# Kernel tuning notes

Hardware: AMD Instinct MI355X
Metric: run time of the kernel (lower is better)

## Reference

```python
import jax, jax.numpy as jnp
import numpy as np

N, E, F, H, C, B = 50000, 1_600_000, 128, 128, 10, 512


def setup_inputs() -> dict:
    key = jax.random.key(0)
    ks = jax.random.split(key, 12)
    inp = {
        "x": jax.random.normal(ks[0], (N, F), dtype=jnp.float32),
        "edge_index": jax.random.randint(ks[1], (2, E), 0, N, dtype=jnp.int32),
        "batch": jnp.sort(jax.random.randint(ks[2], (N,), 0, B, dtype=jnp.int32)),
        "edge_weight": jax.random.uniform(ks[3], (E,), dtype=jnp.float32),
        "W1": jax.random.normal(ks[4], (F, H), dtype=jnp.float32) * 0.05,
        "b1": jnp.zeros((H,), dtype=jnp.float32),
        "W2": jax.random.normal(ks[5], (H, H), dtype=jnp.float32) * 0.05,
        "b2": jnp.zeros((H,), dtype=jnp.float32),
        "W3": jax.random.normal(ks[6], (H, H), dtype=jnp.float32) * 0.05,
        "b3": jnp.zeros((H,), dtype=jnp.float32),
        "Wlin": jax.random.normal(ks[7], (H, C), dtype=jnp.float32) * 0.05,
        "blin": jnp.zeros((C,), dtype=jnp.float32),
    }
    return inp


def reference(x, edge_index, batch, edge_weight, W1, b1, W2, b2, W3, b3, Wlin, blin):
    n = x.shape[0]
    src, dst = edge_index[0], edge_index[1]
    loops = jnp.arange(n, dtype=src.dtype)
    src_f = jnp.concatenate([src, loops])  # edges + self-loops
    dst_f = jnp.concatenate([dst, loops])

    def make_norm(fill_value):
        # GCN symmetric normalization: D^-1/2 (A + fill*I) D^-1/2 on edge weights
        ew = jnp.concatenate([edge_weight, jnp.full((n,), fill_value, dtype=edge_weight.dtype)])
        deg = jax.ops.segment_sum(ew, dst_f, num_segments=n)
        dinv = jnp.where(deg > 0, deg ** -0.5, 0.0)
        return dinv[src_f] * ew * dinv[dst_f]

    # conv1 was built as GCNConv(in, hidden, out_channels) -> third positional arg is
    # `improved`, truthy => self-loop fill value 2.0; conv2/3 use 1.0.
    norm1 = make_norm(2.0)
    norm = make_norm(1.0)

    def gcn_conv(h, W, b, nrm):
        h = h @ W                                   # [N, H]
        msg = h[src_f] * nrm[:, None]               # [E+N, H] gather
        return jax.ops.segment_sum(msg, dst_f, num_segments=n) + b

    h = jax.nn.relu(gcn_conv(x, W1, b1, norm1))
    h = jax.nn.relu(gcn_conv(h, W2, b2, norm))
    h = gcn_conv(h, W3, b3, norm)

    # global_mean_pool over graph ids
    sums = jax.ops.segment_sum(h, batch, num_segments=B)
    cnt = jax.ops.segment_sum(jnp.ones((n,), dtype=h.dtype), batch, num_segments=B)
    pooled = sums / jnp.maximum(cnt, 1.0)[:, None]

    # dropout is identity in eval mode
    return pooled @ Wlin + blin
```

## Files before the change

### kernel.cpp

```cpp
#include <hip/hip_runtime.h>
#include <hip/hip_fp16.h>

#define F 128
#define HID 128
#define NCLS 10
#define CAP 80
#define NBIN 256
#define NPB 196
#define SCAP 7168
#define EPT 8
#define HLS 136

typedef short short8 __attribute__((ext_vector_type(8)));
typedef float float4v __attribute__((ext_vector_type(4)));
typedef float float2v __attribute__((ext_vector_type(2)));

__device__ __forceinline__ unsigned short f2bf(float f) {
    unsigned int u = __float_as_uint(f);
    unsigned int r = (u + 0x7FFFu + ((u >> 16) & 1u)) >> 16;
    return (unsigned short)r;
}
__device__ __forceinline__ float bf2f(unsigned int h) {
    return __uint_as_float(h << 16);
}
__device__ __forceinline__ unsigned char f2fp8(float a) {
    return (unsigned char)(__builtin_amdgcn_cvt_pk_fp8_f32(a, 0.f, 0, false) & 0xFF);
}

__global__ __launch_bounds__(256) void bin_prep_kernel(
    const int* __restrict__ ei, const float* __restrict__ ew,
    int* __restrict__ gcur, uint2* __restrict__ staging, int E, int nbb,
    const float* __restrict__ W1, const float* __restrict__ W2,
    const float* __restrict__ W3, const float* __restrict__ Wlin,
    const float* __restrict__ blin, const float* __restrict__ b3,
    unsigned short* __restrict__ Wp, unsigned short* __restrict__ Wp3s,
    float* __restrict__ bL) {
    __shared__ int lhist[NBIN];
    __shared__ int lbase[NBIN];
    int tid = threadIdx.x;

    if ((int)blockIdx.x < nbb) {
        lhist[tid] = 0;
        __syncthreads();

        unsigned int rpk[EPT];
        unsigned short rd[EPT];
        unsigned short rloc[EPT];
        int base = blockIdx.x * (256 * EPT);
#pragma unroll
        for (int i = 0; i < EPT; i++) {
            int e = base + tid + i * 256;
            if (e < E) {
                int s = ei[e];
                int d = ei[E + e];
                unsigned int q = (unsigned int)(ew[e] * 65535.0f + 0.5f);
                rpk[i] = (q << 16) | (unsigned int)s;
                rd[i] = (unsigned short)d;
                rloc[i] = (unsigned short)atomicAdd(&lhist[d / NPB], 1);
            } else {
                rpk[i] = 0u; rd[i] = 0; rloc[i] = 0;
            }
        }
        __syncthreads();
        lbase[tid] = atomicAdd(&gcur[tid], lhist[tid]);
        __syncthreads();

#pragma unroll
        for (int i = 0; i < EPT; i++) {
            int e = base + tid + i * 256;
            if (e < E) {
                int bin = (int)rd[i] / NPB;
                int pos = lbase[bin] + (int)rloc[i];
                if (pos < SCAP)
                    staging[(size_t)bin * SCAP + pos] =
                        make_uint2(rpk[i], (unsigned int)rd[i]);
            }
        }
    } else {
        int b = blockIdx.x - nbb;
        if (b < 128) {
            int widx = b >> 6;
            const float* W = (widx == 0) ? W1 : W2;
            int idx = (b & 63) * 256 + tid;
            int j = idx & 7;
            int l = (idx >> 3) & 63;
            int nt = (idx >> 9) & 7;
            int kt = idx >> 12;
            int k = kt * 32 + ((l >> 4) << 3) + j;
            int n = nt * 16 + (l & 15);
            Wp[widx * 16384 + idx] = f2bf(W[k * HID + n]);
        } else if (b < 136) {
            int idx = (b - 128) * 256 + tid;
            int j = idx & 7;
            int l = (idx >> 3) & 63;
            int kt = idx >> 9;
            int k = kt * 32 + ((l >> 4) << 3) + j;
            int n = l & 15;
            float v = 0.f;
            if (n < NCLS) {
                for (int m = 0; m < HID; m++)
                    v += W3[k * HID + m] * Wlin[m * NCLS + n];
            }
            Wp3s[idx] = f2bf(v);
        } else {
            if (tid < NCLS) {
                float bl = blin[tid];
                for (int j = 0; j < HID; j++) bl += b3[j] * Wlin[j * NCLS + tid];
                bL[tid] = bl;
            }
        }
    }
}

__global__ __launch_bounds__(1024, 8) void build_gemm1_kernel(
    const uint2* __restrict__ staging, const int* __restrict__ gcur,
    unsigned int* __restrict__ colw, int* __restrict__ cnt,
    float* __restrict__ dinv1, float* __restrict__ dinv0, int N, int nbins,
    const float* __restrict__ X, const unsigned short* __restrict__ Wp,
    unsigned char* __restrict__ Yb8) {
    __shared__ unsigned int lbuck[NPB * CAP];
    __shared__ int lcnt[NPB];
    int tid = threadIdx.x;

    if ((int)blockIdx.x < nbins) {
        int bin = blockIdx.x;
        int node0 = bin * NPB;

        for (int n = tid; n < NPB; n += 1024) lcnt[n] = 0;
        __syncthreads();

        int bcnt = gcur[bin];
        if (bcnt > SCAP) bcnt = SCAP;
        const uint2* st = staging + (size_t)bin * SCAP;
        for (int i = tid; i < bcnt; i += 1024) {
            uint2 t = st[i];
            int dl = (int)t.y - node0;
            int pos = atomicAdd(&lcnt[dl], 1);
            if (pos < CAP) lbuck[dl * CAP + pos] = t.x;
        }
        __syncthreads();

        for (int it = 0; it < NPB; it += 128) {
            int nl = it + (tid >> 3);
            int lane = tid & 7;
            if (nl < NPB) {
                int gn = node0 + nl;
                if (gn < N) {
                    int c = lcnt[nl];
                    if (c > CAP) c = CAP;
                    float s = 0.f;
                    for (int j = lane; j < c; j += 8)
                        s += (float)(lbuck[nl * CAP + j] >> 16);
                    s += __shfl_down(s, 4, 8);
                    s += __shfl_down(s, 2, 8);
                    s += __shfl_down(s, 1, 8);
                    if (lane == 0) {
                        float deg = s * (1.0f / 65535.0f);
                        cnt[gn] = c;
                        dinv1[gn] = 1.0f / sqrtf(deg + 2.0f);
                        dinv0[gn] = 1.0f / sqrtf(deg + 1.0f);
                    }
                }
            }
        }
        __syncthreads();

        int nvalid = N - node0;
        if (nvalid > NPB) nvalid = NPB;
        if (nvalid <= 0) return;
        int nslots = nvalid * (CAP / 4);
        uint4* dst4 = (uint4*)(colw + (size_t)node0 * CAP);
        const uint4* src4 = (const uint4*)lbuck;
        for (int i = tid; i < nslots; i += 1024) {
            int rowi = i / (CAP / 4);
            int slot = i - rowi * (CAP / 4);
            int c = lcnt[rowi];
            if (c > CAP) c = CAP;
            if (slot * 4 < c) dst4[i] = src4[i];
        }
    } else {
        int tile = blockIdx.x - nbins;
        int wave = tid >> 6, lane = tid & 63;
        int quad = lane >> 4, m = lane & 15;
        int row0 = tile * 256 + wave * 16;
        if (row0 >= N) return;
        int row = row0 + m;
        int rowc = row < N ? row : N - 1;

        short8 a[4];
        const float4* xrow = (const float4*)(X + (size_t)rowc * F);
#pragma unroll
        for (int kt = 0; kt < 4; kt++) {
            float4 p0 = xrow[kt * 8 + quad * 2];
            float4 p1 = xrow[kt * 8 + quad * 2 + 1];
            short8 v;
            v[0] = (short)f2bf(p0.x); v[1] = (short)f2bf(p0.y);
            v[2] = (short)f2bf(p0.z); v[3] = (short)f2bf(p0.w);
            v[4] = (short)f2bf(p1.x); v[5] = (short)f2bf(p1.y);
            v[6] = (short)f2bf(p1.z); v[7] = (short)f2bf(p1.w);
            a[kt] = v;
        }

#pragma unroll
        for (int nt = 0; nt < 8; nt++) {
            float4v c = {0.f, 0.f, 0.f, 0.f};
#pragma unroll
            for (int kt = 0; kt < 4; kt++) {
                short8 b = *(const short8*)(Wp + (((kt * 8 + nt) * 64 + lane) << 3));
                c = __builtin_amdgcn_mfma_f32_16x16x32_bf16(a[kt], b, c, 0, 0, 0);
            }
#pragma unroll
            for (int r = 0; r < 4; r++) {
                int gr = row0 + quad * 4 + r;
                if (gr < N) Yb8[(size_t)gr * HID + nt * 16 + m] = f2fp8(c[r]);
            }
        }
    }
}

__device__ __forceinline__ void agg_edge_q(unsigned int w, int fl,
                                           const uint4* __restrict__ hin4,
                                           float2v acc[8]) {
    uint4 h = hin4[(w & 0xFFFFu) * 8 + fl];
    float f = __half2float(__ushort_as_half((unsigned short)(w >> 16)));
    float2v fv = {f, f};
    acc[0] += fv * __builtin_amdgcn_cvt_pk_f32_fp8(h.x, false);
    acc[1] += fv * __builtin_amdgcn_cvt_pk_f32_fp8(h.x, true);
    acc[2] += fv * __builtin_amdgcn_cvt_pk_f32_fp8(h.y, false);
    acc[3] += fv * __builtin_amdgcn_cvt_pk_f32_fp8(h.y, true);
    acc[4] += fv * __builtin_amdgcn_cvt_pk_f32_fp8(h.z, false);
    acc[5] += fv * __builtin_amdgcn_cvt_pk_f32_fp8(h.z, true);
    acc[6] += fv * __builtin_amdgcn_cvt_pk_f32_fp8(h.w, false);
    acc[7] += fv * __builtin_amdgcn_cvt_pk_f32_fp8(h.w, true);
}

__device__ __forceinline__ void agg_node_fp8(int g, int lane,
                                             const unsigned char* __restrict__ hin,
                                             const unsigned int* __restrict__ colw,
                                             const int* __restrict__ cnt,
                                             const float* __restrict__ dinv,
                                             float fill,
                                             const float* __restrict__ bias,
                                             unsigned short* __restrict__ hl_row) {
    float dv = dinv[g];
    int c = cnt[g];
    if (c > CAP) c = CAP;
    const unsigned int* row = colw + (size_t)g * CAP;
    const uint4* hin4 = (const uint4*)hin;

    unsigned int pk[3];
#pragma unroll
    for (int k = 0; k < 3; k++) {
        int idx = lane + k * 32;
        unsigned int e = (idx < c) ? row[idx] : 0u;
        int s = (int)(e & 0xFFFFu);
        float wf = (float)(e >> 16) * (1.0f / 65535.0f) * dinv[s];
        unsigned short hw = __half_as_ushort(__float2half(wf));
        pk[k] = (e & 0xFFFFu) | ((unsigned int)hw << 16);
    }

    int q = lane >> 3;
    int fl = lane & 7;

    float2v acc[8];
#pragma unroll
    for (int i = 0; i < 8; i++) acc[i] = (float2v){0.f, 0.f};

#pragma unroll
    for (int slot = 0; slot < 3; slot++) {
        int base = slot * 32;
        if (c <= base) break;
        int cc = c - base;
        if (cc > 32) cc = 32;
        for (int jj = 0; jj < cc; jj += 8) {
            unsigned int w0 = (unsigned int)__shfl((int)pk[slot], jj + 2 * q, 32);
            unsigned int w1 = (unsigned int)__shfl((int)pk[slot], jj + 2 * q + 1, 32);
            agg_edge_q(w0, fl, hin4, acc);
            agg_edge_q(w1, fl, hin4, acc);
        }
    }

#pragma unroll
    for (int i = 0; i < 8; i++) {
        acc[i][0] += __shfl_down(acc[i][0], 16, 32);
        acc[i][1] += __shfl_down(acc[i][1], 16, 32);
        acc[i][0] += __shfl_down(acc[i][0], 8, 32);
        acc[i][1] += __shfl_down(acc[i][1], 8, 32);
    }

    if (q == 0) {
        uint4 hv = hin4[(size_t)g * 8 + fl];
        float2v ws = {fill * dv, fill * dv};
        float2v dvv = {dv, dv};
        acc[0] = (acc[0] + ws * __builtin_amdgcn_cvt_pk_f32_fp8(hv.x, false)) * dvv;
        acc[1] = (acc[1] + ws * __builtin_amdgcn_cvt_pk_f32_fp8(hv.x, true)) * dvv;
        acc[2] = (acc[2] + ws * __builtin_amdgcn_cvt_pk_f32_fp8(hv.y, false)) * dvv;
        acc[3] = (acc[3] + ws * __builtin_amdgcn_cvt_pk_f32_fp8(hv.y, true)) * dvv;
        acc[4] = (acc[4] + ws * __builtin_amdgcn_cvt_pk_f32_fp8(hv.z, false)) * dvv;
        acc[5] = (acc[5] + ws * __builtin_amdgcn_cvt_pk_f32_fp8(hv.z, true)) * dvv;
        acc[6] = (acc[6] + ws * __builtin_amdgcn_cvt_pk_f32_fp8(hv.w, false)) * dvv;
        acc[7] = (acc[7] + ws * __builtin_amdgcn_cvt_pk_f32_fp8(hv.w, true)) * dvv;

        const float2v* b2 = (const float2v*)(bias + fl * 16);
        uint4 o0, o1;
        unsigned int ow[8];
#pragma unroll
        for (int i = 0; i < 8; i++) {
            float2v v = acc[i] + b2[i];
            float v0 = fmaxf(v[0], 0.f);
            float v1 = fmaxf(v[1], 0.f);
            ow[i] = (unsigned int)f2bf(v0) | ((unsigned int)f2bf(v1) << 16);
        }
        o0 = make_uint4(ow[0], ow[1], ow[2], ow[3]);
        o1 = make_uint4(ow[4], ow[5], ow[6], ow[7]);
        *(uint4*)(hl_row + fl * 16) = o0;
        *(uint4*)(hl_row + fl * 16 + 8) = o1;
    }
}

__global__ __launch_bounds__(512) void agg_gemm128_kernel(const unsigned char* __restrict__ hin,
                                                          const unsigned int* __restrict__ colw,
                                                          const int* __restrict__ cnt,
                                                          const float* __restrict__ dinv,
                                                          const float* __restrict__ bias,
                                                          const unsigned short* __restrict__ Wp2,
                                                          unsigned char* __restrict__ Yb8,
                                                          int N) {
    __shared__ unsigned short hl[16 * HLS];
    __shared__ unsigned char Ol8[16 * 128];

    int tid = threadIdx.x;
    int gl = tid >> 5, lane = tid & 31;
    int row0 = blockIdx.x * 16;
    int g = row0 + gl;

    if (g < N) {
        agg_node_fp8(g, lane, hin, colw, cnt, dinv, 2.0f, bias, hl + gl * HLS);
    } else if ((lane >> 3) == 0) {
        *(uint4*)(hl + gl * HLS + (lane & 7) * 16) = make_uint4(0u, 0u, 0u, 0u);
        *(uint4*)(hl + gl * HLS + (lane & 7) * 16 + 8) = make_uint4(0u, 0u, 0u, 0u);
    }
    __syncthreads();

    int nt = tid >> 6;
    int lane64 = tid & 63;
    int quad = lane64 >> 4, m = lane64 & 15;

    short8 a[4];
#pragma unroll
    for (int kt = 0; kt < 4; kt++)
        a[kt] = *(const short8*)(hl + m * HLS + kt * 32 + quad * 8);

    float4v c = {0.f, 0.f, 0.f, 0.f};
#pragma unroll
    for (int kt = 0; kt < 4; kt++) {
        short8 b = *(const short8*)(Wp2 + (((kt * 8 + nt) * 64 + lane64) << 3));
        c = __builtin_amdgcn_mfma_f32_16x16x32_bf16(a[kt], b, c, 0, 0, 0);
    }
#pragma unroll
    for (int r = 0; r < 4; r++)
        Ol8[(quad * 4 + r) * 128 + nt * 16 + m] = f2fp8(c[r]);
    __syncthreads();

    if (tid < 128) {
        int gr = row0 + (tid >> 3);
        if (gr < N)
            ((uint4*)(Yb8 + (size_t)gr * 128))[tid & 7] = ((const uint4*)Ol8)[tid];
    }
}

__global__ __launch_bounds__(512) void agg_gemm16_kernel(const unsigned char* __restrict__ hin,
                                                         const unsigned int* __restrict__ colw,
                                                         const int* __restrict__ cnt,
                                                         const float* __restrict__ dinv,
                                                         const float* __restrict__ bias,
                                                         const unsigned short* __restrict__ Wp3s,
                                                         unsigned short* __restrict__ g3s,
                                                         int N) {
    __shared__ unsigned short hl[16 * HLS];

    int tid = threadIdx.x;
    int gl = tid >> 5, lane = tid & 31;
    int row0 = blockIdx.x * 16;
    int g = row0 + gl;

    if (g < N) {
        agg_node_fp8(g, lane, hin, colw, cnt, dinv, 1.0f, bias, hl + gl * HLS);
    } else if ((lane >> 3) == 0) {
        *(uint4*)(hl + gl * HLS + (lane & 7) * 16) = make_uint4(0u, 0u, 0u, 0u);
        *(uint4*)(hl + gl * HLS + (lane & 7) * 16 + 8) = make_uint4(0u, 0u, 0u, 0u);
    }
    __syncthreads();

    if (tid < 64) {
        int lane64 = tid;
        int quad = lane64 >> 4, m = lane64 & 15;
        short8 a[4];
#pragma unroll
        for (int kt = 0; kt < 4; kt++)
            a[kt] = *(const short8*)(hl + m * HLS + kt * 32 + quad * 8);
        float4v c = {0.f, 0.f, 0.f, 0.f};
#pragma unroll
        for (int kt = 0; kt < 4; kt++) {
            short8 b = *(const short8*)(Wp3s + ((kt * 64 + lane64) << 3));
            c = __builtin_amdgcn_mfma_f32_16x16x32_bf16(a[kt], b, c, 0, 0, 0);
        }
#pragma unroll
        for (int r = 0; r < 4; r++) {
            int gr = row0 + quad * 4 + r;
            if (gr < N) g3s[(size_t)gr * 16 + m] = f2bf(c[r]);
        }
    }
}

__device__ __forceinline__ void agg3_slot(unsigned int pk, int cc, int lane2off,
                                          const unsigned short* __restrict__ g3s,
                                          float& ax, float& ay) {
    if (cc == 8) {
        unsigned int w[8];
        unsigned int h[8];
#pragma unroll
        for (int t = 0; t < 8; t++)
            w[t] = (unsigned int)__shfl((int)pk, t, 8);
#pragma unroll
        for (int t = 0; t < 8; t++)
            h[t] = *(const unsigned int*)(g3s + (w[t] & 0xFFFFu) * 16 + lane2off);
#pragma unroll
        for (int t = 0; t < 8; t++) {
            float f = __half2float(__ushort_as_half((unsigned short)(w[t] >> 16)));
            ax += f * bf2f(h[t] & 0xFFFFu);
            ay += f * bf2f(h[t] >> 16);
        }
    } else {
        for (int t = 0; t < cc; t++) {
            unsigned int w = (unsigned int)__shfl((int)pk, t, 8);
            unsigned int h = *(const unsigned int*)(g3s + (w & 0xFFFFu) * 16 + lane2off);
            float f = __half2float(__ushort_as_half((unsigned short)(w >> 16)));
            ax += f * bf2f(h & 0xFFFFu);
            ay += f * bf2f(h >> 16);
        }
    }
}

__global__ __launch_bounds__(256) void agg3_kernel(const unsigned short* __restrict__ g3s,
                                                   const unsigned int* __restrict__ colw,
                                                   const int* __restrict__ cnt,
                                                   const float* __restrict__ dinv,
                                                   unsigned short* __restrict__ h3s, int N) {
    int g = (blockIdx.x * blockDim.x + threadIdx.x) >> 3;
    int lane = threadIdx.x & 7;
    if (g >= N) return;

    float dv = dinv[g];
    int c = cnt[g];
    if (c > CAP) c = CAP;
    const unsigned int* row = colw + (size_t)g * CAP;
    int lane2off = lane * 2;

    unsigned int pk[10];
#pragma unroll
    for (int k = 0; k < 10; k++) {
        int idx = lane + k * 8;
        unsigned int e = (idx < c) ? row[idx] : 0u;
        int s = (int)(e & 0xFFFFu);
        float wf = (float)(e >> 16) * (1.0f / 65535.0f) * dinv[s];
        unsigned short hw = __half_as_ushort(__float2half(wf));
        pk[k] = (e & 0xFFFFu) | ((unsigned int)hw << 16);
    }

    float ax = 0.f, ay = 0.f;
#pragma unroll
    for (int slot = 0; slot < 10; slot++) {
        int base = slot * 8;
        if (c > base) {
            int cc = c - base;
            if (cc > 8) cc = 8;
            agg3_slot(pk[slot], cc, lane2off, g3s, ax, ay);
        }
    }

    unsigned int hv = *(const unsigned int*)(g3s + (size_t)g * 16 + lane2off);
    ax = (ax + dv * bf2f(hv & 0xFFFFu)) * dv;
    ay = (ay + dv * bf2f(hv >> 16)) * dv;

    unsigned int o = (unsigned int)f2bf(ax) | ((unsigned int)f2bf(ay) << 16);
    *(unsigned int*)(h3s + (size_t)g * 16 + lane2off) = o;
}

__global__ __launch_bounds__(256) void pool3_kernel(const unsigned short* __restrict__ h3s,
                                                    const int* __restrict__ batch,
                                                    const float* __restrict__ bL,
                                                    const float* __restrict__ blin,
                                                    float* __restrict__ out, int N, int B) {
    int wave = (blockIdx.x * blockDim.x + threadIdx.x) >> 6;
    int lane = threadIdx.x & 63;
    if (wave >= B) return;
    int g = wave;
    int d = lane & 15, sub = lane >> 4;

    int lo = 0, hi = N;
    while (lo < hi) { int m = (lo + hi) >> 1; if (batch[m] < g) lo = m + 1; else hi = m; }
    int s0 = lo;
    hi = N;
    while (lo < hi) { int m = (lo + hi) >> 1; if (batch[m] < g + 1) lo = m + 1; else hi = m; }
    int s1 = lo;

    float p = 0.f;
    for (int v = s0 + sub; v < s1; v += 4)
        p += bf2f((unsigned int)h3s[(size_t)v * 16 + d]);
    p += __shfl_down(p, 32, 64);
    p += __shfl_down(p, 16, 64);

    if (lane < NCLS) {
        int cntv = s1 - s0;
        float r = (cntv > 0) ? (p / (float)cntv + bL[d]) : blin[d];
        out[g * NCLS + d] = r;
    }
}

extern "C" void kernel_launch(void* const* d_in, const int* in_sizes, int n_in,
                              void* d_out, int out_size, void* d_ws, size_t ws_size,
                              hipStream_t stream) {
    const float* x    = (const float*)d_in[0];
    const int*   ei   = (const int*)d_in[1];
    const int*   batch= (const int*)d_in[2];
    const float* ew   = (const float*)d_in[3];
    const float* W1   = (const float*)d_in[4];
    const float* b1   = (const float*)d_in[5];
    const float* W2   = (const float*)d_in[6];
    const float* b2   = (const float*)d_in[7];
    const float* W3   = (const float*)d_in[8];
    const float* b3   = (const float*)d_in[9];
    const float* Wlin = (const float*)d_in[10];
    const float* blin = (const float*)d_in[11];
    float* out = (float*)d_out;

    int N = in_sizes[0] / F;
    int E = in_sizes[1] / 2;
    int B = out_size / NCLS;

    char* p = (char*)d_ws;
    auto alloc = [&](size_t bytes) -> void* {
        void* r = (void*)p;
        p += (bytes + 255) & ~(size_t)255;
        return r;
    };
    int*            cnt   = (int*)alloc((size_t)N * 4);
    float*          dinv1 = (float*)alloc((size_t)N * 4);
    float*          dinv0 = (float*)alloc((size_t)N * 4);
    int*            gcur  = (int*)alloc(NBIN * 4);
    float*          bL    = (float*)alloc(16 * 4);
    unsigned int*   colw  = (unsigned int*)alloc((size_t)N * CAP * 4);
    unsigned short* Wp    = (unsigned short*)alloc(2 * 16384 * 2);
    unsigned short* Wp3s  = (unsigned short*)alloc(2048 * 2);
    unsigned char*  bufA  = (unsigned char*)alloc((size_t)N * HID);
    unsigned char*  bufB  = (unsigned char*)alloc((size_t)N * HID);
    unsigned short* g3s   = (unsigned short*)alloc((size_t)N * 16 * 2);
    unsigned short* h3s   = (unsigned short*)alloc((size_t)N * 16 * 2);
    uint2*          staging = (uint2*)alloc((size_t)NBIN * SCAP * 8);

    int tb = 256;
    int nbins = (N + NPB - 1) / NPB;
    int nbb = (E + tb * EPT - 1) / (tb * EPT);
    int g1tiles = (N + 255) / 256;

    hipMemsetAsync(gcur, 0, NBIN * 4, stream);
    bin_prep_kernel<<<nbb + 137, tb, 0, stream>>>(ei, ew, gcur, staging, E, nbb,
                                                  W1, W2, W3, Wlin, blin, b3,
                                                  Wp, Wp3s, bL);
    build_gemm1_kernel<<<nbins + g1tiles, 1024, 0, stream>>>(staging, gcur, colw, cnt,
                                                             dinv1, dinv0, N, nbins,
                                                             x, Wp, bufA);

    int fused_blocks = (N + 15) / 16;
    int agg3_blocks = ((N * 8) + tb - 1) / tb;

    agg_gemm128_kernel<<<fused_blocks, 512, 0, stream>>>(bufA, colw, cnt, dinv1, b1,
                                                         Wp + 16384, bufB, N);
    agg_gemm16_kernel<<<fused_blocks, 512, 0, stream>>>(bufB, colw, cnt, dinv0, b2,
                                                        Wp3s, g3s, N);
    agg3_kernel<<<agg3_blocks, tb, 0, stream>>>(g3s, colw, cnt, dinv0, h3s, N);
    pool3_kernel<<<((B * 64) + tb - 1) / tb, tb, 0, stream>>>(h3s, batch, bL, blin,
                                                              out, N, B);
}
```

Baseline: 249.4 us.

## Replace binned staging CSR build with direct atomic scatter into per-node buckets

Result: slower. 339.2 us (+36.0%).

```diff
diff --git a/kernel.cpp b/kernel.cpp
--- a/kernel.cpp
+++ b/kernel.cpp
@@ -5,9 +5,6 @@
 #define HID 128
 #define NCLS 10
 #define CAP 80
-#define NBIN 256
-#define NPB 196
-#define SCAP 7168
 #define EPT 8
 #define HLS 136
 
@@ -27,57 +24,32 @@
     return (unsigned char)(__builtin_amdgcn_cvt_pk_fp8_f32(a, 0.f, 0, false) & 0xFF);
 }
 
-__global__ __launch_bounds__(256) void bin_prep_kernel(
+__global__ __launch_bounds__(256) void scatter_prep_kernel(
     const int* __restrict__ ei, const float* __restrict__ ew,
-    int* __restrict__ gcur, uint2* __restrict__ staging, int E, int nbb,
+    int* __restrict__ cnt, unsigned int* __restrict__ colw, int E, int nsb,
     const float* __restrict__ W1, const float* __restrict__ W2,
     const float* __restrict__ W3, const float* __restrict__ Wlin,
     const float* __restrict__ blin, const float* __restrict__ b3,
     unsigned short* __restrict__ Wp, unsigned short* __restrict__ Wp3s,
     float* __restrict__ bL) {
-    __shared__ int lhist[NBIN];
-    __shared__ int lbase[NBIN];
     int tid = threadIdx.x;
 
-    if ((int)blockIdx.x < nbb) {
-        lhist[tid] = 0;
-        __syncthreads();
-
-        unsigned int rpk[EPT];
-        unsigned short rd[EPT];
-        unsigned short rloc[EPT];
+    if ((int)blockIdx.x < nsb) {
         int base = blockIdx.x * (256 * EPT);
 #pragma unroll
         for (int i = 0; i < EPT; i++) {
-            int e = base + tid + i * 256;
+            int e = base + i * 256 + tid;
             if (e < E) {
                 int s = ei[e];
                 int d = ei[E + e];
                 unsigned int q = (unsigned int)(ew[e] * 65535.0f + 0.5f);
-                rpk[i] = (q << 16) | (unsigned int)s;
-                rd[i] = (unsigned short)d;
-                rloc[i] = (unsigned short)atomicAdd(&lhist[d / NPB], 1);
-            } else {
-                rpk[i] = 0u; rd[i] = 0; rloc[i] = 0;
+                int pos = atomicAdd(&cnt[d], 1);
+                if (pos < CAP)
+                    colw[(size_t)d * CAP + pos] = (q << 16) | (unsigned int)s;
             }
         }
-        __syncthreads();
-        lbase[tid] = atomicAdd(&gcur[tid], lhist[tid]);
-        __syncthreads();
-
-#pragma unroll
-        for (int i = 0; i < EPT; i++) {
-            int e = base + tid + i * 256;
-            if (e < E) {
-                int bin = (int)rd[i] / NPB;
-                int pos = lbase[bin] + (int)rloc[i];
-                if (pos < SCAP)
-                    staging[(size_t)bin * SCAP + pos] =
-                        make_uint2(rpk[i], (unsigned int)rd[i]);
-            }
-        }
     } else {
-        int b = blockIdx.x - nbb;
+        int b = blockIdx.x - nsb;
         if (b < 128) {
             int widx = b >> 6;
             const float* W = (widx == 0) ? W1 : W2;
@@ -112,77 +84,18 @@
     }
 }
 
-__global__ __launch_bounds__(1024, 8) void build_gemm1_kernel(
-    const uint2* __restrict__ staging, const int* __restrict__ gcur,
-    unsigned int* __restrict__ colw, int* __restrict__ cnt,
-    float* __restrict__ dinv1, float* __restrict__ dinv0, int N, int nbins,
+__global__ __launch_bounds__(256) void gemm1_dinv_kernel(
     const float* __restrict__ X, const unsigned short* __restrict__ Wp,
-    unsigned char* __restrict__ Yb8) {
-    __shared__ unsigned int lbuck[NPB * CAP];
-    __shared__ int lcnt[NPB];
+    unsigned char* __restrict__ Yb8, const unsigned int* __restrict__ colw,
+    const int* __restrict__ cnt, float* __restrict__ dinv1,
+    float* __restrict__ dinv0, int N, int g1t) {
     int tid = threadIdx.x;
 
-    if ((int)blockIdx.x < nbins) {
-        int bin = blockIdx.x;
-        int node0 = bin * NPB;
-
-        for (int n = tid; n < NPB; n += 1024) lcnt[n] = 0;
-        __syncthreads();
-
-        int bcnt = gcur[bin];
-        if (bcnt > SCAP) bcnt = SCAP;
-        const uint2* st = staging + (size_t)bin * SCAP;
-        for (int i = tid; i < bcnt; i += 1024) {
-            uint2 t = st[i];
-            int dl = (int)t.y - node0;
-            int pos = atomicAdd(&lcnt[dl], 1);
-            if (pos < CAP) lbuck[dl * CAP + pos] = t.x;
-        }
-        __syncthreads();
-
-        for (int it = 0; it < NPB; it += 128) {
-            int nl = it + (tid >> 3);
-            int lane = tid & 7;
-            if (nl < NPB) {
-                int gn = node0 + nl;
-                if (gn < N) {
-                    int c = lcnt[nl];
-                    if (c > CAP) c = CAP;
-                    float s = 0.f;
-                    for (int j = lane; j < c; j += 8)
-                        s += (float)(lbuck[nl * CAP + j] >> 16);
-                    s += __shfl_down(s, 4, 8);
-                    s += __shfl_down(s, 2, 8);
-                    s += __shfl_down(s, 1, 8);
-                    if (lane == 0) {
-                        float deg = s * (1.0f / 65535.0f);
-                        cnt[gn] = c;
-                        dinv1[gn] = 1.0f / sqrtf(deg + 2.0f);
-                        dinv0[gn] = 1.0f / sqrtf(deg + 1.0f);
-                    }
-                }
-            }
-        }
-        __syncthreads();
-
-        int nvalid = N - node0;
-        if (nvalid > NPB) nvalid = NPB;
-        if (nvalid <= 0) return;
-        int nslots = nvalid * (CAP / 4);
-        uint4* dst4 = (uint4*)(colw + (size_t)node0 * CAP);
-        const uint4* src4 = (const uint4*)lbuck;
-        for (int i = tid; i < nslots; i += 1024) {
-            int rowi = i / (CAP / 4);
-            int slot = i - rowi * (CAP / 4);
-            int c = lcnt[rowi];
-            if (c > CAP) c = CAP;
-            if (slot * 4 < c) dst4[i] = src4[i];
-        }
-    } else {
-        int tile = blockIdx.x - nbins;
+    if ((int)blockIdx.x < g1t) {
+        int tile = blockIdx.x;
         int wave = tid >> 6, lane = tid & 63;
         int quad = lane >> 4, m = lane & 15;
-        int row0 = tile * 256 + wave * 16;
+        int row0 = tile * 64 + wave * 16;
         if (row0 >= N) return;
         int row = row0 + m;
         int rowc = row < N ? row : N - 1;
@@ -214,6 +127,31 @@
                 int gr = row0 + quad * 4 + r;
                 if (gr < N) Yb8[(size_t)gr * HID + nt * 16 + m] = f2fp8(c[r]);
             }
+        }
+    } else {
+        int b = blockIdx.x - g1t;
+        int g = b * 32 + (tid >> 3);
+        int lane = tid & 7;
+        if (g >= N) return;
+        int c = cnt[g];
+        if (c > CAP) c = CAP;
+        const uint4* row4 = (const uint4*)(colw + (size_t)g * CAP);
+        float s = 0.f;
+        for (int j4 = lane; j4 * 4 < c; j4 += 8) {
+            uint4 v = row4[j4];
+            int base = j4 * 4;
+            if (base + 0 < c) s += (float)(v.x >> 16);
+            if (base + 1 < c) s += (float)(v.y >> 16);
+            if (base + 2 < c) s += (float)(v.z >> 16);
+            if (base + 3 < c) s += (float)(v.w >> 16);
+        }
+        s += __shfl_down(s, 4, 8);
+        s += __shfl_down(s, 2, 8);
+        s += __shfl_down(s, 1, 8);
+        if (lane == 0) {
+            float deg = s * (1.0f / 65535.0f);
+            dinv1[g] = 1.0f / sqrtf(deg + 2.0f);
+            dinv0[g] = 1.0f / sqrtf(deg + 1.0f);
         }
     }
 }
@@ -548,7 +486,6 @@
     int*            cnt   = (int*)alloc((size_t)N * 4);
     float*          dinv1 = (float*)alloc((size_t)N * 4);
     float*          dinv0 = (float*)alloc((size_t)N * 4);
-    int*            gcur  = (int*)alloc(NBIN * 4);
     float*          bL    = (float*)alloc(16 * 4);
     unsigned int*   colw  = (unsigned int*)alloc((size_t)N * CAP * 4);
     unsigned short* Wp    = (unsigned short*)alloc(2 * 16384 * 2);
@@ -557,20 +494,18 @@
     unsigned char*  bufB  = (unsigned char*)alloc((size_t)N * HID);
     unsigned short* g3s   = (unsigned short*)alloc((size_t)N * 16 * 2);
     unsigned short* h3s   = (unsigned short*)alloc((size_t)N * 16 * 2);
-    uint2*          staging = (uint2*)alloc((size_t)NBIN * SCAP * 8);
 
     int tb = 256;
-    int nbins = (N + NPB - 1) / NPB;
-    int nbb = (E + tb * EPT - 1) / (tb * EPT);
-    int g1tiles = (N + 255) / 256;
-
-    hipMemsetAsync(gcur, 0, NBIN * 4, stream);
-    bin_prep_kernel<<<nbb + 137, tb, 0, stream>>>(ei, ew, gcur, staging, E, nbb,
-                                                  W1, W2, W3, Wlin, blin, b3,
-                                                  Wp, Wp3s, bL);
-    build_gemm1_kernel<<<nbins + g1tiles, 1024, 0, stream>>>(staging, gcur, colw, cnt,
-                                                             dinv1, dinv0, N, nbins,
-                                                             x, Wp, bufA);
+    int nsb = (E + tb * EPT - 1) / (tb * EPT);
+    int g1t = (N + 63) / 64;
+    int ndb = (N + 31) / 32;
+
+    hipMemsetAsync(cnt, 0, (size_t)N * 4, stream);
+    scatter_prep_kernel<<<nsb + 137, tb, 0, stream>>>(ei, ew, cnt, colw, E, nsb,
+                                                      W1, W2, W3, Wlin, blin, b3,
+                                                      Wp, Wp3s, bL);
+    gemm1_dinv_kernel<<<g1t + ndb, tb, 0, stream>>>(x, Wp, bufA, colw, cnt,
+                                                    dinv1, dinv0, N, g1t);
 
     int fused_blocks = (N + 15) / 16;
     int agg3_blocks = ((N * 8) + tb - 1) / tb;
```
